# Performance work log

Hardware: AMD Instinct MI355X
Metric: run time of the kernel (lower is better)

Reference implementation:

```python
import jax, jax.numpy as jnp
from jax import lax
import numpy as np

STRIDES = (8.0, 16.0, 32.0)
SIZES = ((256, 256), (128, 128), (64, 64))  # HxW per level for a 2048x2048 input
C = 80            # num_classes
TOPK = 1000       # topk_candidates per level
CONF = 0.05       # conf_thresh
NMS_T = 0.6       # nms_thresh
OFFSET = 1.0e5    # class offset for multiclass (class-aware) NMS


def _anchors(H, W, stride):
    ys, xs = jnp.meshgrid(jnp.arange(H, dtype=jnp.float32),
                          jnp.arange(W, dtype=jnp.float32), indexing='ij')
    a = jnp.stack([xs, ys], axis=-1).reshape(-1, 2)  # [M,2] (x,y)
    return (a + 0.5) * stride


def _level(obj, cls, reg, H, W, stride):
    # decode boxes: ctr = reg[:, :2]*s + anchor; wh = exp(reg[:, 2:])*s
    anc = _anchors(H, W, stride)
    ctr = reg[:, :2] * stride + anc
    wh = jnp.exp(reg[:, 2:]) * stride
    boxes = jnp.concatenate([ctr - 0.5 * wh, ctr + 0.5 * wh], axis=-1)  # [M,4]
    # fused score: sqrt(sigmoid(obj) * sigmoid(cls)), flattened over (M, C)
    scores = jnp.sqrt(jax.nn.sigmoid(obj) * jax.nn.sigmoid(cls)).reshape(-1)  # [M*C]
    k = min(TOPK, boxes.shape[0])
    top_scores, top_idx = lax.top_k(scores, k)  # == sort(desc)[:k]
    anchor_idx = top_idx // C
    labels = top_idx % C
    return boxes[anchor_idx], top_scores, labels


def _iou_matrix(b):
    x1, y1, x2, y2 = b[:, 0], b[:, 1], b[:, 2], b[:, 3]
    area = jnp.maximum(x2 - x1, 0.0) * jnp.maximum(y2 - y1, 0.0)
    xx1 = jnp.maximum(x1[:, None], x1[None, :])
    yy1 = jnp.maximum(y1[:, None], y1[None, :])
    xx2 = jnp.minimum(x2[:, None], x2[None, :])
    yy2 = jnp.minimum(y2[:, None], y2[None, :])
    inter = jnp.maximum(xx2 - xx1, 0.0) * jnp.maximum(yy2 - yy1, 0.0)
    return inter / (area[:, None] + area[None, :] - inter + 1e-10)


def setup_inputs() -> dict:
    key = jax.random.key(0)
    ks = jax.random.split(key, 9)
    inp = {}
    names = ['obj0', 'cls0', 'reg0', 'obj1', 'cls1', 'reg1', 'obj2', 'cls2', 'reg2']
    shapes = [(65536, 1), (65536, C), (65536, 4),
              (16384, 1), (16384, C), (16384, 4),
              (4096, 1), (4096, C), (4096, 4)]
    for n, s, k in zip(names, shapes, ks):
        inp[n] = jax.random.normal(k, s, dtype=jnp.float32)
    return inp


def reference(obj0, cls0, reg0, obj1, cls1, reg1, obj2, cls2, reg2):
    levels = [(obj0, cls0, reg0), (obj1, cls1, reg1), (obj2, cls2, reg2)]
    bs, ss, ls = [], [], []
    for (o, c, r), (H, W), s in zip(levels, SIZES, STRIDES):
        b, sc, lb = _level(o, c, r, H, W, s)
        bs.append(b); ss.append(sc); ls.append(lb)
    boxes = jnp.concatenate(bs, axis=0)   # [N,4], N = 3*TOPK
    scores = jnp.concatenate(ss, axis=0)  # [N]
    labels = jnp.concatenate(ls, axis=0)  # [N] int

    # global sort by score desc (NMS order)
    order = jnp.argsort(-scores)
    b = boxes[order]; sc = scores[order]; lb = labels[order]

    # class-aware NMS via per-class coordinate offset
    b_off = b + (lb.astype(jnp.float32) * OFFSET)[:, None]
    iou = _iou_matrix(b_off)  # [N,N]

    N = sc.shape[0]
    idx = jnp.arange(N)
    keep0 = sc > CONF  # conf_thresh gating; below-thresh never suppress

    def body(i, keep):
        sup = (iou[i] > NMS_T) & (idx > i) & keep[i]
        return keep & (~sup)

    keep = lax.fori_loop(0, N, body, keep0)
    # fixed-shape outputs: suppressed / below-threshold detections get score 0
    return b, jnp.where(keep, sc, 0.0), lb
```

## Files before the change

### kernel.cpp

```cpp
#include <hip/hip_runtime.h>
#include <cstdint>
#include <math.h>

#define C_CLS      80
#define TOPK       1000
#define NCAND      3000
#define OFFSET_F   100000.0f
#define FLOOR_BITS 0x3F333333u
#define NBINS      512
#define CAP        8192
#define MASK_W     48
#define NBLK       47
#define RTILE      2048
#define ITILE      16
#define CAPB0      57344
#define CAPB1      49152
#define CAPB2      32768
#define FBIN0      154u
#define FBIN1      103u
#define FBIN2      52u
#define STGB       1024
#define SLICE      375

static __device__ __forceinline__ float np_expf(float x) {
    const float magic = 12582912.0f;
    float q = fmaf(x, 1.442695040888963407359924681e+00f, magic);
    q = q - magic;
    float r = fmaf(q, -6.93145752e-1f, x);
    r = fmaf(q, -1.428606765330187045e-06f, r);
    float p = fmaf(r, 5.082762527590693718096e-04f, 6.757896990527504603057e-03f);
    p = fmaf(p, r, 5.114512081637298353406e-02f);
    p = fmaf(p, r, 2.473615434895520810817e-01f);
    p = fmaf(p, r, 7.257664613233124478488e-01f);
    p = fmaf(p, r, 9.999999999980870924916e-01f);
    float d = fmaf(r, 2.159509375685829852307e-02f, -2.742335390411667452936e-01f);
    d = fmaf(d, r, 1.0f);
    float e = p / d;
    int qi = (int)q;
    return __uint_as_float(__float_as_uint(e) + ((unsigned int)qi << 23));
}

static __device__ __forceinline__ float sigmoid_np(float x) {
    float e = np_expf(-x);
    return 1.0f / (1.0f + e);
}

__global__ void sweep_kernel(const float* __restrict__ c0, const float* __restrict__ c1,
                             const float* __restrict__ c2,
                             const float* __restrict__ o0, const float* __restrict__ o1,
                             const float* __restrict__ o2,
                             unsigned int* __restrict__ hist, unsigned int* __restrict__ meta,
                             unsigned long long* __restrict__ buf_all) {
    __shared__ unsigned int h[NBINS];
    __shared__ unsigned long long stg[STGB];
    __shared__ float s_sig[56], s_flo[56];
    __shared__ unsigned int scnt, srb;

    int bb = blockIdx.x;
    const float *cls, *obj; int base, lvl;
    if (bb < 1280)      { lvl = 0; cls = c0; obj = o0; base = bb * 4096; }
    else if (bb < 1600) { lvl = 1; cls = c1; obj = o1; base = (bb - 1280) * 4096; }
    else                { lvl = 2; cls = c2; obj = o2; base = (bb - 1600) * 4096; }
    const unsigned int fbin = (lvl == 0) ? FBIN0 : (lvl == 1) ? FBIN1 : FBIN2;
    const unsigned int Fb   = FLOOR_BITS + (fbin << 14);
    unsigned long long* buf = buf_all + ((lvl == 0) ? 0 : (lvl == 1) ? CAPB0 : (CAPB0 + CAPB1));
    const unsigned int capl = (lvl == 0) ? CAPB0 : (lvl == 1) ? CAPB1 : CAPB2;
    unsigned int* mcnt = &meta[lvl * 4];

    float4 cv[4];
    #pragma unroll
    for (int it = 0; it < 4; ++it)
        cv[it] = *(const float4*)(cls + base + it * 1024 + threadIdx.x * 4);

    for (int i = threadIdx.x; i < NBINS; i += 256) h[i] = 0;
    if (threadIdx.x == 0) scnt = 0;
    int a0 = base / C_CLS;
    int nA = (base + 4095) / C_CLS - a0 + 1;
    float F2f = __uint_as_float(Fb); F2f = F2f * F2f;
    if (threadIdx.x < nA) {
        float sig = sigmoid_np(obj[a0 + threadIdx.x]);
        s_sig[threadIdx.x] = sig;
        float q = F2f / fmaxf(sig, 1e-30f);
        s_flo[threadIdx.x] = (q >= 0.9999f) ? 9.18f : (__logf(q) - __logf(1.0f - q) - 0.03f);
    }
    __syncthreads();

    #pragma unroll
    for (int it = 0; it < 4; ++it) {
        int e = base + it * 1024 + threadIdx.x * 4;
        float c4[4] = {cv[it].x, cv[it].y, cv[it].z, cv[it].w};
        #pragma unroll
        for (int k = 0; k < 4; ++k) {
            int ee = e + k;
            int ai = ee / C_CLS - a0;
            float c = c4[k];
            if (c >= s_flo[ai]) {
                float s = sqrtf(s_sig[ai] * sigmoid_np(c));
                unsigned int bits = __float_as_uint(s);
                if (bits >= Fb) {
                    atomicAdd(&h[(bits - FLOOR_BITS) >> 14], 1u);
                    unsigned long long key = ((unsigned long long)bits << 32) |
                                             (unsigned long long)(0xFFFFFFFFu - (unsigned int)ee);
                    unsigned int pos = atomicAdd(&scnt, 1u);
                    if (pos < STGB) stg[pos] = key;
                    else {
                        unsigned int gp = atomicAdd(mcnt, 1u);
                        if (gp < capl) buf[gp] = key;
                    }
                }
            }
        }
    }
    __syncthreads();
    unsigned int n = scnt; if (n > STGB) n = STGB;
    if (threadIdx.x == 0 && n) srb = atomicAdd(mcnt, n);
    __syncthreads();
    if (n) {
        unsigned int rb = srb;
        for (unsigned int i = threadIdx.x; i < n; i += 256) {
            unsigned int dst = rb + i;
            if (dst < capl) buf[dst] = stg[i];
        }
    }
    unsigned int* ho = hist + lvl * NBINS;
    for (int i = threadIdx.x; i < NBINS; i += 256)
        if (h[i]) atomicAdd(&ho[i], h[i]);
}

__global__ void collectB_kernel(const unsigned long long* __restrict__ buf_all,
                                const unsigned int* __restrict__ hist,
                                unsigned int* __restrict__ meta,
                                unsigned long long* __restrict__ cand_all) {
    __shared__ unsigned int sh[NBINS];
    __shared__ unsigned int sT;
    int lvl = blockIdx.y;
    for (int i = threadIdx.x; i < NBINS; i += 256) sh[i] = hist[lvl * NBINS + i];
    __syncthreads();
    if (threadIdx.x == 0) {
        unsigned int cum = 0; int B = 0;
        for (int b = 320; b >= 0; --b) {
            cum += sh[b];
            if (cum >= TOPK) { B = b; break; }
        }
        sT = FLOOR_BITS + ((unsigned int)B << 14);
    }
    __syncthreads();
    const unsigned int T = sT;
    const unsigned long long* buf = buf_all + ((lvl == 0) ? 0 : (lvl == 1) ? CAPB0 : (CAPB0 + CAPB1));
    unsigned int capl = (lvl == 0) ? CAPB0 : (lvl == 1) ? CAPB1 : CAPB2;
    unsigned int m = meta[lvl * 4]; if (m > capl) m = capl;
    unsigned long long* cand = cand_all + (size_t)lvl * CAP;
    for (unsigned int i = blockIdx.x * 256 + threadIdx.x; i < m; i += 16 * 256) {
        unsigned long long e = buf[i];
        if ((unsigned int)(e >> 32) >= T) {
            unsigned int pos = atomicAdd(&meta[lvl * 4 + 1], 1u);
            if (pos < CAP) cand[pos] = e;
        }
    }
}

__global__ void rank_kernel(const unsigned long long* __restrict__ cand_all,
                            const unsigned int* __restrict__ meta,
                            float* __restrict__ sel_score, unsigned int* __restrict__ sel_anchor,
                            unsigned int* __restrict__ sel_label) {
    __shared__ unsigned long long tile[RTILE];
    int lvl = blockIdx.y;
    const unsigned long long* cand = cand_all + (size_t)lvl * CAP;
    unsigned int m = meta[lvl * 4 + 1]; if (m > CAP) m = CAP;
    if ((unsigned int)(blockIdx.x * 256) >= m) return;
    int t = blockIdx.x * 256 + threadIdx.x;
    bool live = (unsigned int)t < m;
    unsigned long long key = live ? cand[t] : 0ull;
    int r = 0;
    for (unsigned int base = 0; base < m; base += RTILE) {
        unsigned int n = m - base; if (n > RTILE) n = RTILE;
        __syncthreads();
        for (unsigned int i = threadIdx.x; i < n; i += 256) tile[i] = cand[base + i];
        __syncthreads();
        if (live) {
            #pragma unroll 8
            for (unsigned int j = 0; j < n; ++j) r += (tile[j] > key);
        }
    }
    if (live && r < TOPK) {
        unsigned int bits = (unsigned int)(key >> 32);
        unsigned int ee   = 0xFFFFFFFFu - (unsigned int)key;
        int slot = lvl * TOPK + r;
        sel_score[slot]  = __uint_as_float(bits);
        sel_anchor[slot] = ee / C_CLS;
        sel_label[slot]  = ee % C_CLS;
    }
}

__global__ void build_sort_kernel(const float* __restrict__ reg0, const float* __restrict__ reg1,
                                  const float* __restrict__ reg2,
                                  const float* __restrict__ sel_score,
                                  const unsigned int* __restrict__ sel_anchor,
                                  const unsigned int* __restrict__ sel_label,
                                  float* __restrict__ out, float* __restrict__ sc_sorted,
                                  float* __restrict__ boff) {
    __shared__ unsigned long long keys[NCAND];
    for (int i = threadIdx.x; i < NCAND; i += 256) {
        unsigned int b = __float_as_uint(sel_score[i]);
        keys[i] = ((unsigned long long)b << 12) | (unsigned int)(4095 - i);
    }
    __syncthreads();
    const int gl = threadIdx.x >> 3;
    const int s  = threadIdx.x & 7;
    const int g  = blockIdx.x * 32 + gl;
    if (g >= NCAND) return;
    const unsigned long long kg = keys[g];
    int r = 0;
    const int j0 = s * SLICE;
    #pragma unroll 8
    for (int i = 0; i < SLICE; ++i) r += (keys[j0 + i] > kg);
    r += __shfl_down(r, 4, 8);
    r += __shfl_down(r, 2, 8);
    r += __shfl_down(r, 1, 8);
    if (s != 0) return;
    int lvl = g / TOPK;
    unsigned int a   = sel_anchor[g];
    unsigned int lab = sel_label[g];
    const float* reg = (lvl == 0) ? reg0 : (lvl == 1) ? reg1 : reg2;
    int   W      = (lvl == 0) ? 256 : (lvl == 1) ? 128 : 64;
    float stride = (lvl == 0) ? 8.0f : (lvl == 1) ? 16.0f : 32.0f;
    float4 rv = *(const float4*)(reg + (size_t)a * 4);
    float ax = ((float)(a % W) + 0.5f) * stride;
    float ay = ((float)(a / W) + 0.5f) * stride;
    float cx = rv.x * stride + ax;
    float cy = rv.y * stride + ay;
    float wx = np_expf(rv.z) * stride;
    float wy = np_expf(rv.w) * stride;
    float x1 = cx - 0.5f * wx, y1 = cy - 0.5f * wy;
    float x2 = cx + 0.5f * wx, y2 = cy + 0.5f * wy;
    out[r * 4 + 0] = x1; out[r * 4 + 1] = y1; out[r * 4 + 2] = x2; out[r * 4 + 3] = y2;
    sc_sorted[r] = sel_score[g];
    out[15000 + r] = (float)lab;
    float off = (float)lab * OFFSET_F;
    boff[r * 4 + 0] = x1 + off; boff[r * 4 + 1] = y1 + off;
    boff[r * 4 + 2] = x2 + off; boff[r * 4 + 3] = y2 + off;
}

__global__ void mask_kernel(const float* __restrict__ boff, unsigned long long* __restrict__ mask,
                            unsigned long long* __restrict__ diag,
                            unsigned long long* __restrict__ rnz) {
    #pragma clang fp contract(off)
    __shared__ float4 bis[ITILE];
    int i0 = blockIdx.y * ITILE;
    if (threadIdx.x < ITILE) {
        int ir = i0 + threadIdx.x; if (ir >= NCAND) ir = NCAND - 1;
        bis[threadIdx.x] = *(const float4*)(boff + (size_t)ir * 4);
    }
    __syncthreads();
    int j = blockIdx.x * 256 + threadIdx.x;
    float4 bj = {0, 0, 0, 0};
    if (j < NCAND) bj = *(const float4*)(boff + (size_t)j * 4);
    float aj = fmaxf(bj.z - bj.x, 0.0f) * fmaxf(bj.w - bj.y, 0.0f);
    int wslot = blockIdx.x * 4 + (threadIdx.x >> 6);
    #pragma unroll
    for (int ii = 0; ii < ITILE; ++ii) {
        int i = i0 + ii;
        float4 bi = bis[ii];
        bool pred = false;
        if (j < NCAND && j > i) {
            float ai = fmaxf(bi.z - bi.x, 0.0f) * fmaxf(bi.w - bi.y, 0.0f);
            float xx1 = fmaxf(bi.x, bj.x);
            float yy1 = fmaxf(bi.y, bj.y);
            float xx2 = fminf(bi.z, bj.z);
            float yy2 = fminf(bi.w, bj.w);
            float inter = fmaxf(xx2 - xx1, 0.0f) * fmaxf(yy2 - yy1, 0.0f);
            float u = ai + aj;
            u = u - inter;
            u = u + 1e-10f;
            float iou = inter / u;
            pred = (double)iou > 0.6;
        }
        unsigned long long bal = __ballot(pred);
        if ((threadIdx.x & 63) == 0 && i < NCAND) {
            mask[(size_t)i * MASK_W + wslot] = bal;
            if (wslot == (i >> 6)) diag[i] = bal;
            if (bal) atomicOr(&rnz[i >> 6], 1ull << (i & 63));
        }
    }
}

__global__ void __launch_bounds__(64) nms_reduce(const unsigned long long* __restrict__ mask,
                                                 const unsigned long long* __restrict__ diag,
                                                 const unsigned long long* __restrict__ rnzmap,
                                                 const float* __restrict__ sc,
                                                 float* __restrict__ out_sc) {
    int t = threadIdx.x;
    unsigned long long confw = 0ull;
    if (t < NBLK) {
        #pragma unroll 8
        for (int j = 0; j < 64; ++j) {
            int g = t * 64 + j;
            if (g < NCAND && (double)sc[g] > 0.05) confw |= 1ull << j;
        }
    }
    unsigned long long rnz_t = (t < NBLK) ? rnzmap[t] : 0ull;
    unsigned long long supp = 0ull, keepw = 0ull;
    unsigned long long Dcur  = diag[t];
    unsigned long long Dnext = diag[64 + t];
    for (int b = 0; b < NBLK; ++b) {
        unsigned long long Dfut = (b + 2 < NBLK) ? diag[(size_t)(b + 2) * 64 + t] : 0ull;
        unsigned long long confb = __shfl(confw, b);
        unsigned long long suppb = __shfl(supp, b);
        unsigned long long rnzb  = __shfl(rnz_t, b);
        unsigned long long res = confb & ~suppb;
        unsigned long long work = res & rnzb;
        while (work) {
            int k = __builtin_ctzll(work);
            res &= ~__shfl(Dcur, k);
            work = res & rnzb & ((k == 63) ? 0ull : (~0ull << (k + 1)));
        }
        if (t == b) keepw = res;
        unsigned long long app = res & rnzb;
        while (app) {
            int k = __builtin_ctzll(app);
            app &= app - 1;
            if (t < MASK_W) supp |= mask[(size_t)(64 * b + k) * MASK_W + t];
        }
        Dcur = Dnext; Dnext = Dfut;
    }
    if (t < NBLK) {
        #pragma unroll 8
        for (int j = 0; j < 64; ++j) {
            int g = t * 64 + j;
            if (g < NCAND) out_sc[g] = ((keepw >> j) & 1ull) ? sc[g] : 0.0f;
        }
    }
}

extern "C" void kernel_launch(void* const* d_in, const int* in_sizes, int n_in,
                              void* d_out, int out_size, void* d_ws, size_t ws_size,
                              hipStream_t stream) {
    const float* o0 = (const float*)d_in[0];
    const float* c0 = (const float*)d_in[1];
    const float* r0 = (const float*)d_in[2];
    const float* o1 = (const float*)d_in[3];
    const float* c1 = (const float*)d_in[4];
    const float* r1 = (const float*)d_in[5];
    const float* o2 = (const float*)d_in[6];
    const float* c2 = (const float*)d_in[7];
    const float* r2 = (const float*)d_in[8];
    float* out = (float*)d_out;
    char*  ws  = (char*)d_ws;

    unsigned int*       hist       = (unsigned int*)(ws + 0);
    unsigned long long* rnz        = (unsigned long long*)(ws + 6144);
    unsigned int*       meta       = (unsigned int*)(ws + 6528);
    unsigned long long* cand       = (unsigned long long*)(ws + 6592);
    float*              sel_score  = (float*)(ws + 203200);
    unsigned int*       sel_anchor = (unsigned int*)(ws + 215200);
    unsigned int*       sel_label  = (unsigned int*)(ws + 227200);
    float*              sc_sorted  = (float*)(ws + 239200);
    float*              boff       = (float*)(ws + 251200);
    unsigned long long* mask       = (unsigned long long*)(ws + 299200);
    unsigned long long* diag       = (unsigned long long*)(ws + 1454272);
    unsigned long long* fbuf       = (unsigned long long*)(ws + 299200);

    hipMemsetAsync(hist, 0, 6592, stream);

    sweep_kernel<<<1680, 256, 0, stream>>>(c0, c1, c2, o0, o1, o2, hist, meta, fbuf);

    collectB_kernel<<<dim3(16, 3), 256, 0, stream>>>(fbuf, hist, meta, cand);

    rank_kernel<<<dim3(CAP / 256, 3), 256, 0, stream>>>(cand, meta, sel_score, sel_anchor, sel_label);

    build_sort_kernel<<<94, 256, 0, stream>>>(r0, r1, r2, sel_score, sel_anchor, sel_label,
                                              out, sc_sorted, boff);

    mask_kernel<<<dim3(12, 188), 256, 0, stream>>>(boff, mask, diag, rnz);

    nms_reduce<<<1, 64, 0, stream>>>(mask, diag, rnz, sc_sorted, out + 12000);
}
```

Before: 198.4 us.

## Fuse post-sweep stages into one cooperative kernel with grid syncs

Merges the threshold/collect, rank, build/sort, IoU mask and NMS reduce kernels into a single cooperative kernel launched with 256 blocks, separating the phases with grid-wide syncs. The aim is to remove per-launch overhead and the inter-kernel gaps of four launches. The collect phase now spreads over more blocks, while the mask phase loops over its tiles with fewer blocks. Each phase boundary now pays a grid barrier, and the work is tied to the cooperative co-residency limits.

```diff
diff --git a/kernel.cpp b/kernel.cpp
--- a/kernel.cpp
+++ b/kernel.cpp
@@ -1,6 +1,9 @@
 #include <hip/hip_runtime.h>
+#include <hip/hip_cooperative_groups.h>
 #include <cstdint>
 #include <math.h>
+
+namespace cg = cooperative_groups;
 
 #define C_CLS      80
 #define TOPK       1000
@@ -11,7 +14,6 @@
 #define CAP        8192
 #define MASK_W     48
 #define NBLK       47
-#define RTILE      2048
 #define ITILE      16
 #define CAPB0      57344
 #define CAPB1      49152
@@ -21,6 +23,7 @@
 #define FBIN2      52u
 #define STGB       1024
 #define SLICE      375
+#define TAILB      256
 
 static __device__ __forceinline__ float np_expf(float x) {
     const float magic = 12582912.0f;
@@ -127,207 +130,228 @@
         if (h[i]) atomicAdd(&ho[i], h[i]);
 }
 
-__global__ void collectB_kernel(const unsigned long long* __restrict__ buf_all,
-                                const unsigned int* __restrict__ hist,
-                                unsigned int* __restrict__ meta,
-                                unsigned long long* __restrict__ cand_all) {
-    __shared__ unsigned int sh[NBINS];
-    __shared__ unsigned int sT;
-    int lvl = blockIdx.y;
-    for (int i = threadIdx.x; i < NBINS; i += 256) sh[i] = hist[lvl * NBINS + i];
-    __syncthreads();
-    if (threadIdx.x == 0) {
-        unsigned int cum = 0; int B = 0;
-        for (int b = 320; b >= 0; --b) {
-            cum += sh[b];
-            if (cum >= TOPK) { B = b; break; }
-        }
-        sT = FLOOR_BITS + ((unsigned int)B << 14);
-    }
-    __syncthreads();
-    const unsigned int T = sT;
-    const unsigned long long* buf = buf_all + ((lvl == 0) ? 0 : (lvl == 1) ? CAPB0 : (CAPB0 + CAPB1));
-    unsigned int capl = (lvl == 0) ? CAPB0 : (lvl == 1) ? CAPB1 : CAPB2;
-    unsigned int m = meta[lvl * 4]; if (m > capl) m = capl;
-    unsigned long long* cand = cand_all + (size_t)lvl * CAP;
-    for (unsigned int i = blockIdx.x * 256 + threadIdx.x; i < m; i += 16 * 256) {
-        unsigned long long e = buf[i];
-        if ((unsigned int)(e >> 32) >= T) {
-            unsigned int pos = atomicAdd(&meta[lvl * 4 + 1], 1u);
-            if (pos < CAP) cand[pos] = e;
-        }
-    }
-}
-
-__global__ void rank_kernel(const unsigned long long* __restrict__ cand_all,
-                            const unsigned int* __restrict__ meta,
-                            float* __restrict__ sel_score, unsigned int* __restrict__ sel_anchor,
-                            unsigned int* __restrict__ sel_label) {
-    __shared__ unsigned long long tile[RTILE];
-    int lvl = blockIdx.y;
-    const unsigned long long* cand = cand_all + (size_t)lvl * CAP;
-    unsigned int m = meta[lvl * 4 + 1]; if (m > CAP) m = CAP;
-    if ((unsigned int)(blockIdx.x * 256) >= m) return;
-    int t = blockIdx.x * 256 + threadIdx.x;
-    bool live = (unsigned int)t < m;
-    unsigned long long key = live ? cand[t] : 0ull;
-    int r = 0;
-    for (unsigned int base = 0; base < m; base += RTILE) {
-        unsigned int n = m - base; if (n > RTILE) n = RTILE;
+__global__ void __launch_bounds__(256) tail_kernel(
+    const unsigned long long* __restrict__ fbuf,
+    const unsigned int* __restrict__ hist,
+    unsigned int* __restrict__ meta,
+    unsigned long long* __restrict__ cand,
+    const float* __restrict__ reg0, const float* __restrict__ reg1,
+    const float* __restrict__ reg2,
+    float* __restrict__ sel_score, unsigned int* __restrict__ sel_anchor,
+    unsigned int* __restrict__ sel_label,
+    float* __restrict__ out, float* __restrict__ sc_sorted, float* __restrict__ boff,
+    unsigned long long* __restrict__ mask, unsigned long long* __restrict__ diag,
+    unsigned long long* __restrict__ rnz)
+{
+    cg::grid_group grid = cg::this_grid();
+    __shared__ unsigned long long sm[3072];
+    __shared__ float4 bis[ITILE];
+    __shared__ unsigned int sT[3];
+    const int tid = threadIdx.x;
+    const unsigned int gtid = blockIdx.x * 256u + (unsigned int)tid;
+    const unsigned int gsz  = gridDim.x * 256u;
+
+    {
+        unsigned int* hh = (unsigned int*)sm;
+        for (int lvl = 0; lvl < 3; ++lvl) {
+            for (int i = tid; i < NBINS; i += 256) hh[i] = hist[lvl * NBINS + i];
+            __syncthreads();
+            if (tid == 0) {
+                unsigned int cum = 0; int B = 0;
+                for (int b = 320; b >= 0; --b) {
+                    cum += hh[b];
+                    if (cum >= TOPK) { B = b; break; }
+                }
+                sT[lvl] = FLOOR_BITS + ((unsigned int)B << 14);
+            }
+            __syncthreads();
+        }
+        const unsigned int caps[3] = {CAPB0, CAPB1, CAPB2};
+        const unsigned int offs[3] = {0, CAPB0, CAPB0 + CAPB1};
+        for (int lvl = 0; lvl < 3; ++lvl) {
+            unsigned int m = meta[lvl * 4]; if (m > caps[lvl]) m = caps[lvl];
+            const unsigned long long* bl = fbuf + offs[lvl];
+            unsigned long long* cl = cand + (size_t)lvl * CAP;
+            const unsigned int T = sT[lvl];
+            for (unsigned int i = gtid; i < m; i += gsz) {
+                unsigned long long e = bl[i];
+                if ((unsigned int)(e >> 32) >= T) {
+                    unsigned int p = atomicAdd(&meta[lvl * 4 + 1], 1u);
+                    if (p < CAP) cl[p] = e;
+                }
+            }
+        }
+    }
+    __threadfence();
+    grid.sync();
+
+    if (blockIdx.x < 96) {
+        int lvl = blockIdx.x >> 5;
+        unsigned int m = meta[lvl * 4 + 1]; if (m > CAP) m = CAP;
+        if ((unsigned int)((blockIdx.x & 31) * 256) < m) {
+            const unsigned long long* cl = cand + (size_t)lvl * CAP;
+            int t = (blockIdx.x & 31) * 256 + tid;
+            bool live = (unsigned int)t < m;
+            unsigned long long key = live ? cl[t] : 0ull;
+            int r = 0;
+            for (unsigned int base = 0; base < m; base += 2048) {
+                unsigned int n = m - base; if (n > 2048) n = 2048;
+                __syncthreads();
+                for (unsigned int i = tid; i < n; i += 256) sm[i] = cl[base + i];
+                __syncthreads();
+                if (live) {
+                    #pragma unroll 8
+                    for (unsigned int j = 0; j < n; ++j) r += (sm[j] > key);
+                }
+            }
+            if (live && r < TOPK) {
+                unsigned int bits = (unsigned int)(key >> 32);
+                unsigned int ee   = 0xFFFFFFFFu - (unsigned int)key;
+                int slot = lvl * TOPK + r;
+                sel_score[slot]  = __uint_as_float(bits);
+                sel_anchor[slot] = ee / C_CLS;
+                sel_label[slot]  = ee % C_CLS;
+            }
+        }
+    }
+    __threadfence();
+    grid.sync();
+
+    if (blockIdx.x < 94) {
+        for (int i = tid; i < NCAND; i += 256) {
+            unsigned int b = __float_as_uint(sel_score[i]);
+            sm[i] = ((unsigned long long)b << 12) | (unsigned int)(4095 - i);
+        }
         __syncthreads();
-        for (unsigned int i = threadIdx.x; i < n; i += 256) tile[i] = cand[base + i];
-        __syncthreads();
-        if (live) {
+        const int gl = tid >> 3, s = tid & 7;
+        const int g  = blockIdx.x * 32 + gl;
+        if (g < NCAND) {
+            const unsigned long long kg = sm[g];
+            int r = 0;
+            const int j0 = s * SLICE;
             #pragma unroll 8
-            for (unsigned int j = 0; j < n; ++j) r += (tile[j] > key);
-        }
-    }
-    if (live && r < TOPK) {
-        unsigned int bits = (unsigned int)(key >> 32);
-        unsigned int ee   = 0xFFFFFFFFu - (unsigned int)key;
-        int slot = lvl * TOPK + r;
-        sel_score[slot]  = __uint_as_float(bits);
-        sel_anchor[slot] = ee / C_CLS;
-        sel_label[slot]  = ee % C_CLS;
-    }
-}
-
-__global__ void build_sort_kernel(const float* __restrict__ reg0, const float* __restrict__ reg1,
-                                  const float* __restrict__ reg2,
-                                  const float* __restrict__ sel_score,
-                                  const unsigned int* __restrict__ sel_anchor,
-                                  const unsigned int* __restrict__ sel_label,
-                                  float* __restrict__ out, float* __restrict__ sc_sorted,
-                                  float* __restrict__ boff) {
-    __shared__ unsigned long long keys[NCAND];
-    for (int i = threadIdx.x; i < NCAND; i += 256) {
-        unsigned int b = __float_as_uint(sel_score[i]);
-        keys[i] = ((unsigned long long)b << 12) | (unsigned int)(4095 - i);
-    }
-    __syncthreads();
-    const int gl = threadIdx.x >> 3;
-    const int s  = threadIdx.x & 7;
-    const int g  = blockIdx.x * 32 + gl;
-    if (g >= NCAND) return;
-    const unsigned long long kg = keys[g];
-    int r = 0;
-    const int j0 = s * SLICE;
-    #pragma unroll 8
-    for (int i = 0; i < SLICE; ++i) r += (keys[j0 + i] > kg);
-    r += __shfl_down(r, 4, 8);
-    r += __shfl_down(r, 2, 8);
-    r += __shfl_down(r, 1, 8);
-    if (s != 0) return;
-    int lvl = g / TOPK;
-    unsigned int a   = sel_anchor[g];
-    unsigned int lab = sel_label[g];
-    const float* reg = (lvl == 0) ? reg0 : (lvl == 1) ? reg1 : reg2;
-    int   W      = (lvl == 0) ? 256 : (lvl == 1) ? 128 : 64;
-    float stride = (lvl == 0) ? 8.0f : (lvl == 1) ? 16.0f : 32.0f;
-    float4 rv = *(const float4*)(reg + (size_t)a * 4);
-    float ax = ((float)(a % W) + 0.5f) * stride;
-    float ay = ((float)(a / W) + 0.5f) * stride;
-    float cx = rv.x * stride + ax;
-    float cy = rv.y * stride + ay;
-    float wx = np_expf(rv.z) * stride;
-    float wy = np_expf(rv.w) * stride;
-    float x1 = cx - 0.5f * wx, y1 = cy - 0.5f * wy;
-    float x2 = cx + 0.5f * wx, y2 = cy + 0.5f * wy;
-    out[r * 4 + 0] = x1; out[r * 4 + 1] = y1; out[r * 4 + 2] = x2; out[r * 4 + 3] = y2;
-    sc_sorted[r] = sel_score[g];
-    out[15000 + r] = (float)lab;
-    float off = (float)lab * OFFSET_F;
-    boff[r * 4 + 0] = x1 + off; boff[r * 4 + 1] = y1 + off;
-    boff[r * 4 + 2] = x2 + off; boff[r * 4 + 3] = y2 + off;
-}
-
-__global__ void mask_kernel(const float* __restrict__ boff, unsigned long long* __restrict__ mask,
-                            unsigned long long* __restrict__ diag,
-                            unsigned long long* __restrict__ rnz) {
-    #pragma clang fp contract(off)
-    __shared__ float4 bis[ITILE];
-    int i0 = blockIdx.y * ITILE;
-    if (threadIdx.x < ITILE) {
-        int ir = i0 + threadIdx.x; if (ir >= NCAND) ir = NCAND - 1;
-        bis[threadIdx.x] = *(const float4*)(boff + (size_t)ir * 4);
-    }
-    __syncthreads();
-    int j = blockIdx.x * 256 + threadIdx.x;
-    float4 bj = {0, 0, 0, 0};
-    if (j < NCAND) bj = *(const float4*)(boff + (size_t)j * 4);
-    float aj = fmaxf(bj.z - bj.x, 0.0f) * fmaxf(bj.w - bj.y, 0.0f);
-    int wslot = blockIdx.x * 4 + (threadIdx.x >> 6);
-    #pragma unroll
-    for (int ii = 0; ii < ITILE; ++ii) {
-        int i = i0 + ii;
-        float4 bi = bis[ii];
-        bool pred = false;
-        if (j < NCAND && j > i) {
-            float ai = fmaxf(bi.z - bi.x, 0.0f) * fmaxf(bi.w - bi.y, 0.0f);
-            float xx1 = fmaxf(bi.x, bj.x);
-            float yy1 = fmaxf(bi.y, bj.y);
-            float xx2 = fminf(bi.z, bj.z);
-            float yy2 = fminf(bi.w, bj.w);
-            float inter = fmaxf(xx2 - xx1, 0.0f) * fmaxf(yy2 - yy1, 0.0f);
-            float u = ai + aj;
-            u = u - inter;
-            u = u + 1e-10f;
-            float iou = inter / u;
-            pred = (double)iou > 0.6;
-        }
-        unsigned long long bal = __ballot(pred);
-        if ((threadIdx.x & 63) == 0 && i < NCAND) {
-            mask[(size_t)i * MASK_W + wslot] = bal;
-            if (wslot == (i >> 6)) diag[i] = bal;
-            if (bal) atomicOr(&rnz[i >> 6], 1ull << (i & 63));
-        }
-    }
-}
-
-__global__ void __launch_bounds__(64) nms_reduce(const unsigned long long* __restrict__ mask,
-                                                 const unsigned long long* __restrict__ diag,
-                                                 const unsigned long long* __restrict__ rnzmap,
-                                                 const float* __restrict__ sc,
-                                                 float* __restrict__ out_sc) {
-    int t = threadIdx.x;
-    unsigned long long confw = 0ull;
-    if (t < NBLK) {
-        #pragma unroll 8
-        for (int j = 0; j < 64; ++j) {
-            int g = t * 64 + j;
-            if (g < NCAND && (double)sc[g] > 0.05) confw |= 1ull << j;
-        }
-    }
-    unsigned long long rnz_t = (t < NBLK) ? rnzmap[t] : 0ull;
-    unsigned long long supp = 0ull, keepw = 0ull;
-    unsigned long long Dcur  = diag[t];
-    unsigned long long Dnext = diag[64 + t];
-    for (int b = 0; b < NBLK; ++b) {
-        unsigned long long Dfut = (b + 2 < NBLK) ? diag[(size_t)(b + 2) * 64 + t] : 0ull;
-        unsigned long long confb = __shfl(confw, b);
-        unsigned long long suppb = __shfl(supp, b);
-        unsigned long long rnzb  = __shfl(rnz_t, b);
-        unsigned long long res = confb & ~suppb;
-        unsigned long long work = res & rnzb;
-        while (work) {
-            int k = __builtin_ctzll(work);
-            res &= ~__shfl(Dcur, k);
-            work = res & rnzb & ((k == 63) ? 0ull : (~0ull << (k + 1)));
-        }
-        if (t == b) keepw = res;
-        unsigned long long app = res & rnzb;
-        while (app) {
-            int k = __builtin_ctzll(app);
-            app &= app - 1;
-            if (t < MASK_W) supp |= mask[(size_t)(64 * b + k) * MASK_W + t];
-        }
-        Dcur = Dnext; Dnext = Dfut;
-    }
-    if (t < NBLK) {
-        #pragma unroll 8
-        for (int j = 0; j < 64; ++j) {
-            int g = t * 64 + j;
-            if (g < NCAND) out_sc[g] = ((keepw >> j) & 1ull) ? sc[g] : 0.0f;
+            for (int i = 0; i < SLICE; ++i) r += (sm[j0 + i] > kg);
+            r += __shfl_down(r, 4, 8);
+            r += __shfl_down(r, 2, 8);
+            r += __shfl_down(r, 1, 8);
+            if (s == 0) {
+                int lvl = g / TOPK;
+                unsigned int a   = sel_anchor[g];
+                unsigned int lab = sel_label[g];
+                const float* reg = (lvl == 0) ? reg0 : (lvl == 1) ? reg1 : reg2;
+                int   W      = (lvl == 0) ? 256 : (lvl == 1) ? 128 : 64;
+                float stride = (lvl == 0) ? 8.0f : (lvl == 1) ? 16.0f : 32.0f;
+                float4 rv = *(const float4*)(reg + (size_t)a * 4);
+                float ax = ((float)(a % W) + 0.5f) * stride;
+                float ay = ((float)(a / W) + 0.5f) * stride;
+                float cx = rv.x * stride + ax;
+                float cy = rv.y * stride + ay;
+                float wx = np_expf(rv.z) * stride;
+                float wy = np_expf(rv.w) * stride;
+                float x1 = cx - 0.5f * wx, y1 = cy - 0.5f * wy;
+                float x2 = cx + 0.5f * wx, y2 = cy + 0.5f * wy;
+                out[r * 4 + 0] = x1; out[r * 4 + 1] = y1;
+                out[r * 4 + 2] = x2; out[r * 4 + 3] = y2;
+                sc_sorted[r] = sel_score[g];
+                out[15000 + r] = (float)lab;
+                float off = (float)lab * OFFSET_F;
+                boff[r * 4 + 0] = x1 + off; boff[r * 4 + 1] = y1 + off;
+                boff[r * 4 + 2] = x2 + off; boff[r * 4 + 3] = y2 + off;
+            }
+        }
+    }
+    __threadfence();
+    grid.sync();
+
+    {
+        #pragma clang fp contract(off)
+        for (unsigned int mt = blockIdx.x; mt < 12u * 188u; mt += gridDim.x) {
+            int bx = (int)(mt % 12u), by = (int)(mt / 12u);
+            int i0 = by * ITILE;
+            __syncthreads();
+            if (tid < ITILE) {
+                int ir = i0 + tid; if (ir >= NCAND) ir = NCAND - 1;
+                bis[tid] = *(const float4*)(boff + (size_t)ir * 4);
+            }
+            __syncthreads();
+            int j = bx * 256 + tid;
+            float4 bj = {0, 0, 0, 0};
+            if (j < NCAND) bj = *(const float4*)(boff + (size_t)j * 4);
+            float aj = fmaxf(bj.z - bj.x, 0.0f) * fmaxf(bj.w - bj.y, 0.0f);
+            int wslot = bx * 4 + (tid >> 6);
+            #pragma unroll
+            for (int ii = 0; ii < ITILE; ++ii) {
+                int i = i0 + ii;
+                float4 bi = bis[ii];
+                bool pred = false;
+                if (j < NCAND && j > i) {
+                    float ai = fmaxf(bi.z - bi.x, 0.0f) * fmaxf(bi.w - bi.y, 0.0f);
+                    float xx1 = fmaxf(bi.x, bj.x);
+                    float yy1 = fmaxf(bi.y, bj.y);
+                    float xx2 = fminf(bi.z, bj.z);
+                    float yy2 = fminf(bi.w, bj.w);
+                    float inter = fmaxf(xx2 - xx1, 0.0f) * fmaxf(yy2 - yy1, 0.0f);
+                    float u = ai + aj;
+                    u = u - inter;
+                    u = u + 1e-10f;
+                    float iou = inter / u;
+                    pred = (double)iou > 0.6;
+                }
+                unsigned long long bal = __ballot(pred);
+                if ((tid & 63) == 0 && i < NCAND) {
+                    mask[(size_t)i * MASK_W + wslot] = bal;
+                    if (wslot == (i >> 6)) diag[i] = bal;
+                    if (bal) atomicOr(&rnz[i >> 6], 1ull << (i & 63));
+                }
+            }
+        }
+    }
+    __threadfence();
+    grid.sync();
+
+    if (blockIdx.x == 0 && tid < 64) {
+        const float* sc = sc_sorted;
+        float* out_sc = out + 12000;
+        int t = tid;
+        unsigned long long confw = 0ull;
+        if (t < NBLK) {
+            #pragma unroll 8
+            for (int j = 0; j < 64; ++j) {
+                int g = t * 64 + j;
+                if (g < NCAND && (double)sc[g] > 0.05) confw |= 1ull << j;
+            }
+        }
+        unsigned long long rnz_t = (t < NBLK) ? rnz[t] : 0ull;
+        unsigned long long supp = 0ull, keepw = 0ull;
+        unsigned long long Dcur  = diag[t];
+        unsigned long long Dnext = diag[64 + t];
+        for (int b = 0; b < NBLK; ++b) {
+            unsigned long long Dfut = (b + 2 < NBLK) ? diag[(size_t)(b + 2) * 64 + t] : 0ull;
+            unsigned long long confb = __shfl(confw, b);
+            unsigned long long suppb = __shfl(supp, b);
+            unsigned long long rnzb  = __shfl(rnz_t, b);
+            unsigned long long res = confb & ~suppb;
+            unsigned long long work = res & rnzb;
+            while (work) {
+                int k = __builtin_ctzll(work);
+                res &= ~__shfl(Dcur, k);
+                work = res & rnzb & ((k == 63) ? 0ull : (~0ull << (k + 1)));
+            }
+            if (t == b) keepw = res;
+            unsigned long long app = res & rnzb;
+            while (app) {
+                int k = __builtin_ctzll(app);
+                app &= app - 1;
+                if (t < MASK_W) supp |= mask[(size_t)(64 * b + k) * MASK_W + t];
+            }
+            Dcur = Dnext; Dnext = Dfut;
+        }
+        if (t < NBLK) {
+            #pragma unroll 8
+            for (int j = 0; j < 64; ++j) {
+                int g = t * 64 + j;
+                if (g < NCAND) out_sc[g] = ((keepw >> j) & 1ull) ? sc[g] : 0.0f;
+            }
         }
     }
 }
@@ -364,14 +388,13 @@
 
     sweep_kernel<<<1680, 256, 0, stream>>>(c0, c1, c2, o0, o1, o2, hist, meta, fbuf);
 
-    collectB_kernel<<<dim3(16, 3), 256, 0, stream>>>(fbuf, hist, meta, cand);
-
-    rank_kernel<<<dim3(CAP / 256, 3), 256, 0, stream>>>(cand, meta, sel_score, sel_anchor, sel_label);
-
-    build_sort_kernel<<<94, 256, 0, stream>>>(r0, r1, r2, sel_score, sel_anchor, sel_label,
-                                              out, sc_sorted, boff);
-
-    mask_kernel<<<dim3(12, 188), 256, 0, stream>>>(boff, mask, diag, rnz);
-
-    nms_reduce<<<1, 64, 0, stream>>>(mask, diag, rnz, sc_sorted, out + 12000);
+    void* targs[] = {
+        (void*)&fbuf, (void*)&hist, (void*)&meta, (void*)&cand,
+        (void*)&r0, (void*)&r1, (void*)&r2,
+        (void*)&sel_score, (void*)&sel_anchor, (void*)&sel_label,
+        (void*)&out, (void*)&sc_sorted, (void*)&boff,
+        (void*)&mask, (void*)&diag, (void*)&rnz
+    };
+    hipLaunchCooperativeKernel((const void*)tail_kernel, dim3(TAILB), dim3(256),
+                               targs, 0, stream);
 }
```

After: 399.8 us. 2.02x slower.
